# Kernel tuning notes

Hardware: AMD Instinct MI355X
Metric: run time of the kernel (lower is better)

The kernel has to match this reference:

```python
import jax, jax.numpy as jnp
import numpy as np

D = 1024  # input_size
NORM = 1.0 / np.sqrt(D)


def setup_inputs() -> dict:
    key = jax.random.key(0)
    k_x, k_q, k_k, k_v = jax.random.split(key, 4)
    B, S = 4, 2048
    scale = 1.0 / np.sqrt(D)  # init ~ nn.Linear default magnitude
    return {
        "inputs": jax.random.normal(k_x, (B, S, D), dtype=jnp.float32),
        "Wq": jax.random.uniform(k_q, (D, D), jnp.float32, -scale, scale),
        "Wk": jax.random.uniform(k_k, (D, D), jnp.float32, -scale, scale),
        "Wv": jax.random.uniform(k_v, (D, D), jnp.float32, -scale, scale),
    }


def reference(inputs, Wq, Wk, Wv):
    # nn.Linear(x) = x @ W.T (no bias)
    Q = jnp.einsum("bsd,ed->bse", inputs, Wq)
    K = jnp.einsum("bsd,ed->bse", inputs, Wk)
    V = jnp.einsum("bsd,ed->bse", inputs, Wv)
    attn = jnp.einsum("bqe,bke->bqk", Q, K) * NORM  # [B,S,S]
    attn = jax.nn.softmax(attn, axis=2)
    return jnp.einsum("bqk,bke->bqe", attn, V)
```

## Files before the change

### kernel.cpp

```cpp
#include <hip/hip_runtime.h>

typedef __bf16 bf16_t;
typedef __bf16 bf16x8 __attribute__((ext_vector_type(8)));
typedef __bf16 bf16x4 __attribute__((ext_vector_type(4)));
typedef float  floatx4 __attribute__((ext_vector_type(4)));

__device__ __forceinline__ void gload_lds16(const bf16_t* g, bf16_t* l) {
    __builtin_amdgcn_global_load_lds(
        (const __attribute__((address_space(1))) void*)g,
        (__attribute__((address_space(3))) void*)l,
        16, 0, 0);
}

template <int MODE, typename OutT>
__global__ __launch_bounds__(512, 2) void gemm8p(
    const bf16_t* __restrict__ A, int lda, size_t batchA,
    const bf16_t* __restrict__ B, int ldb, size_t batchB,
    OutT* __restrict__ C, int ldc, size_t batchC,
    bf16_t* __restrict__ C2, int ldc2,
    float* __restrict__ rowsums, int batchR,
    int K, float scale)
{
    extern __shared__ __align__(16) bf16_t smem[];

    A += (size_t)blockIdx.z * batchA;
    B += (size_t)blockIdx.z * batchB;

    const int tid  = threadIdx.x;
    const int wid  = tid >> 6;
    const int lane = tid & 63;
    const int wr   = wid >> 2;
    const int wc   = wid & 3;
    const int lr   = lane & 15;

    const int bm = blockIdx.x * 256;
    const int bn = blockIdx.y * 256;

    const bf16_t* At = A + (size_t)bm * lda;
    const bf16_t* Bt = B + (size_t)bn * ldb;

    const int    c8 = (((lane & 3) ^ ((lane >> 3) & 3)) << 3);
    const size_t ga = (size_t)(wid * 16 + (lane >> 2)) * lda + c8;
    const size_t gb = (size_t)(wid * 16 + (lane >> 2)) * ldb + c8;
    bf16_t* lw = smem + (wid << 9);

    const int slotoff = (((lane >> 4) ^ ((lr >> 1) & 3)) << 3);

    const int NT = K >> 6;

    floatx4 acc[8][4] = {};
    bf16x8 af[4], bq[4];

#define STAGE(sbuf, sreg, tile) do {                                          \
    bf16_t* _l = lw + ((((sbuf) << 2) | (sreg)) << 13);                       \
    const size_t _k = (size_t)(tile) * 64 + ((sreg) & 1) * 32;                \
    if ((sreg) >= 2) {                                                        \
        gload_lds16(Bt + _k + gb, _l);                                        \
        gload_lds16(Bt + _k + gb + (size_t)128 * ldb, _l + 4096);             \
    } else {                                                                  \
        gload_lds16(At + _k + ga, _l);                                        \
        gload_lds16(At + _k + ga + (size_t)128 * lda, _l + 4096);             \
    }                                                                         \
} while (0)

#define LDA_FRAG(buf, kk, row)                                                \
    (*(const bf16x8*)&smem[((((buf) << 2) | (kk)) << 13) + ((row) << 5) + slotoff])
#define LDB_FRAG(buf, kk, row)                                                \
    (*(const bf16x8*)&smem[((((buf) << 2) | (2 + (kk))) << 13) + ((row) << 5) + slotoff])

#define PHASE(buf, kk, mh, RDB, sbuf, sreg, stile, DOVM) do {                 \
    if (RDB) {                                                                \
        _Pragma("unroll")                                                     \
        for (int j = 0; j < 4; ++j)                                           \
            bq[j] = LDB_FRAG(buf, kk, wc * 64 + j * 16 + lr);                 \
    }                                                                         \
    _Pragma("unroll")                                                         \
    for (int i = 0; i < 4; ++i)                                               \
        af[i] = LDA_FRAG(buf, kk, wr * 128 + (mh) * 64 + i * 16 + lr);        \
    STAGE(sbuf, sreg, stile);                                                 \
    if (DOVM) asm volatile("s_waitcnt vmcnt(6)" ::: "memory");                \
    __builtin_amdgcn_s_barrier();                                             \
    __builtin_amdgcn_s_setprio(1);                                            \
    _Pragma("unroll")                                                         \
    for (int i = 0; i < 4; ++i) {                                             \
        _Pragma("unroll")                                                     \
        for (int j = 0; j < 4; ++j)                                           \
            acc[(mh) * 4 + i][j] = __builtin_amdgcn_mfma_f32_16x16x32_bf16(   \
                bq[j], af[i], acc[(mh) * 4 + i][j], 0, 0, 0);                 \
    }                                                                         \
    __builtin_amdgcn_s_setprio(0);                                            \
    __builtin_amdgcn_s_barrier();                                             \
} while (0)

    STAGE(0, 2, 0); STAGE(0, 0, 0); STAGE(0, 3, 0); STAGE(0, 1, 0);
    STAGE(1, 2, 1); STAGE(1, 0, 1); STAGE(1, 3, 1);
    asm volatile("s_waitcnt vmcnt(6)" ::: "memory");
    __builtin_amdgcn_s_barrier();

    for (int kt = 0; kt < NT; kt += 2) {
        int t1 = kt + 1;
        int t2 = kt + 2; if (t2 >= NT) t2 -= NT;
        int t3 = kt + 3; if (t3 >= NT) t3 -= NT;
        PHASE(0, 0, 0, true,  1, 1, t1, false);
        PHASE(0, 0, 1, false, 0, 2, t2, false);
        PHASE(0, 1, 0, true,  0, 0, t2, false);
        PHASE(0, 1, 1, false, 0, 3, t2, true);
        PHASE(1, 0, 0, true,  0, 1, t2, false);
        PHASE(1, 0, 1, false, 1, 2, t3, false);
        PHASE(1, 1, 0, true,  1, 0, t3, false);
        PHASE(1, 1, 1, false, 1, 3, t3, true);
    }
    asm volatile("s_waitcnt vmcnt(0)" ::: "memory");

#undef PHASE
#undef LDA_FRAG
#undef LDB_FRAG
#undef STAGE

    const int cfix = lane & 15;
    const int creg = (lane >> 4) << 2;

    if constexpr (MODE == 1) {
        if (blockIdx.z == 2) {
            #pragma unroll
            for (int mi = 0; mi < 8; ++mi) {
                int mg = bm + wr * 128 + mi * 16 + cfix;
                #pragma unroll
                for (int j = 0; j < 4; ++j) {
                    int ng = bn + wc * 64 + j * 16 + creg;
                    #pragma unroll
                    for (int r = 0; r < 4; ++r)
                        C2[(size_t)(ng + r) * ldc2 + mg] = (bf16_t)acc[mi][j][r];
                }
            }
            return;
        }
        OutT* Cz = C + (size_t)blockIdx.z * batchC;
        #pragma unroll
        for (int mi = 0; mi < 8; ++mi) {
            size_t row = (size_t)(bm + wr * 128 + mi * 16 + cfix);
            #pragma unroll
            for (int j = 0; j < 4; ++j) {
                int col = bn + wc * 64 + j * 16 + creg;
                bf16x4 v;
                #pragma unroll
                for (int r = 0; r < 4; ++r) v[r] = (bf16_t)acc[mi][j][r];
                *(bf16x4*)&Cz[row * (size_t)ldc + col] = v;
            }
        }
    } else {
        OutT* Cz = C + (size_t)blockIdx.z * batchC;
        float* sums = rowsums + (size_t)blockIdx.z * batchR;
        float rs[8] = {};
        #pragma unroll
        for (int mi = 0; mi < 8; ++mi) {
            size_t row = (size_t)(bm + wr * 128 + mi * 16 + cfix);
            #pragma unroll
            for (int j = 0; j < 4; ++j) {
                int col = bn + wc * 64 + j * 16 + creg;
                bf16x4 v;
                #pragma unroll
                for (int r = 0; r < 4; ++r) {
                    v[r] = (bf16_t)__expf(acc[mi][j][r] * scale);
                    rs[mi] += (float)v[r];
                }
                *(bf16x4*)&Cz[row * (size_t)ldc + col] = v;
            }
        }
        #pragma unroll
        for (int mi = 0; mi < 8; ++mi) {
            rs[mi] += __shfl_xor(rs[mi], 16);
            rs[mi] += __shfl_xor(rs[mi], 32);
        }
        if (lane < 16) {
            #pragma unroll
            for (int mi = 0; mi < 8; ++mi)
                atomicAdd(&sums[bm + wr * 128 + mi * 16 + lane], rs[mi]);
        }
    }
}

template <int MODE, int BKT, typename OutT>
__global__ __launch_bounds__(256) void gemm_nt(
    const bf16_t* __restrict__ A, int lda, size_t batchA,
    const bf16_t* __restrict__ B, int ldb, size_t batchB,
    OutT* __restrict__ C, int ldc, size_t batchC,
    bf16_t* __restrict__ C2, int ldc2,
    float* __restrict__ rowsums, int batchR,
    int K, float scale)
{
    constexpr int CH  = BKT / 8;
    constexpr int RPS = 2048 / BKT;
    constexpr int NSHOT = 128 / RPS;

    __shared__ bf16_t sA[128 * BKT];
    __shared__ bf16_t sB[128 * BKT];

    A += (size_t)blockIdx.z * batchA;
    B += (size_t)blockIdx.z * batchB;

    const int tid  = threadIdx.x;
    const int wid  = tid >> 6;
    const int lane = tid & 63;

    const int bm = blockIdx.x * 128;
    const int bn = blockIdx.y * 128;

    const int rr  = tid / CH;
    const int kc8 = (((tid & (CH - 1)) ^ (rr & (CH - 1))) << 3);

    const int wy = (wid >> 1) * 64;
    const int wx = (wid & 1) * 64;
    const int lr = lane & 15;

    floatx4 acc[4][4] = {};

    const bf16_t* pa = A + (size_t)(bm + rr) * lda + kc8;
    const bf16_t* pb = B + (size_t)(bn + rr) * ldb + kc8;
    bf16_t* la = &sA[wid * 512];
    bf16_t* lb = &sB[wid * 512];

    for (int k0 = 0; k0 < K; k0 += BKT) {
        #pragma unroll
        for (int c = 0; c < NSHOT; ++c) {
            gload_lds16(pa + (size_t)(c * RPS) * lda + k0, la + c * 2048);
            gload_lds16(pb + (size_t)(c * RPS) * ldb + k0, lb + c * 2048);
        }
        __syncthreads();

        #pragma unroll
        for (int kk = 0; kk < BKT / 32; ++kk) {
            const int cch = (kk << 2) + (lane >> 4);
            bf16x8 af[4], bqf[4];
            #pragma unroll
            for (int i = 0; i < 4; ++i) {
                int r = wy + i * 16 + lr;
                af[i] = *(const bf16x8*)&sA[r * BKT + ((cch ^ (r & (CH - 1))) << 3)];
            }
            #pragma unroll
            for (int j = 0; j < 4; ++j) {
                int r = wx + j * 16 + lr;
                bqf[j] = *(const bf16x8*)&sB[r * BKT + ((cch ^ (r & (CH - 1))) << 3)];
            }
            #pragma unroll
            for (int i = 0; i < 4; ++i)
                #pragma unroll
                for (int j = 0; j < 4; ++j)
                    acc[i][j] = __builtin_amdgcn_mfma_f32_16x16x32_bf16(
                        bqf[j], af[i], acc[i][j], 0, 0, 0);
        }
        __syncthreads();
    }

    const int cfix = lane & 15;
    const int creg = (lane >> 4) << 2;

    if constexpr (MODE == 3) {
        OutT* Cz = C + (size_t)blockIdx.z * batchC;
        const float* sums = rowsums + (size_t)blockIdx.z * batchR;
        #pragma unroll
        for (int i = 0; i < 4; ++i) {
            int rloc = bm + wy + i * 16 + cfix;
            float rinv = 1.0f / sums[rloc];
            size_t row = (size_t)rloc;
            #pragma unroll
            for (int j = 0; j < 4; ++j) {
                int col = bn + wx + j * 16 + creg;
                floatx4 v;
                #pragma unroll
                for (int r = 0; r < 4; ++r) v[r] = acc[i][j][r] * rinv;
                *(floatx4*)&Cz[row * (size_t)ldc + col] = v;
            }
        }
    }
    (void)C2; (void)ldc2; (void)scale;
}

__global__ __launch_bounds__(256) void cvt_all(
    const float* __restrict__ X, const float* __restrict__ Wq,
    const float* __restrict__ Wk, const float* __restrict__ Wv,
    bf16_t* __restrict__ Xb, bf16_t* __restrict__ Wqb,
    bf16_t* __restrict__ Wkb, bf16_t* __restrict__ Wvb,
    float* __restrict__ sums, int nsums,
    int nX4, int nW4)
{
    int i = blockIdx.x * blockDim.x + threadIdx.x;
    if (i < nsums) sums[i] = 0.f;
    const float* src; bf16_t* dst; int idx;
    if (i < nX4) { src = X; dst = Xb; idx = i; }
    else {
        int j = i - nX4;
        int w = j / nW4;
        idx = j - w * nW4;
        if (i >= nX4 + 3 * nW4) return;
        src = (w == 0) ? Wq : (w == 1) ? Wk : Wv;
        dst = (w == 0) ? Wqb : (w == 1) ? Wkb : Wvb;
    }
    float4 v = ((const float4*)src)[idx];
    bf16x4 o;
    o[0] = (bf16_t)v.x; o[1] = (bf16_t)v.y; o[2] = (bf16_t)v.z; o[3] = (bf16_t)v.w;
    *(bf16x4*)(dst + (size_t)idx * 4) = o;
}

extern "C" void kernel_launch(void* const* d_in, const int* in_sizes, int n_in,
                              void* d_out, int out_size, void* d_ws, size_t ws_size,
                              hipStream_t stream)
{
    (void)in_sizes; (void)n_in; (void)out_size; (void)ws_size;
    const float* X  = (const float*)d_in[0];
    const float* Wq = (const float*)d_in[1];
    const float* Wk = (const float*)d_in[2];
    const float* Wv = (const float*)d_in[3];
    float* out = (float*)d_out;

    const int Bb = 4, S = 2048, D = 1024;
    const int M = Bb * S;

    char* ws = (char*)d_ws;
    size_t off = 0;
    auto carve = [&](size_t bytes) -> char* {
        char* p = ws + off;
        off += (bytes + 255) & ~(size_t)255;
        return p;
    };
    bf16_t* Xb  = (bf16_t*)carve((size_t)M * D * 2);
    bf16_t* Wqb = (bf16_t*)carve((size_t)D * D * 2);
    bf16_t* Wkb = (bf16_t*)carve((size_t)D * D * 2);
    bf16_t* Wvb = (bf16_t*)carve((size_t)D * D * 2);
    bf16_t* Qb  = (bf16_t*)carve((size_t)M * D * 2);
    bf16_t* Kb  = (bf16_t*)carve((size_t)M * D * 2);
    bf16_t* Vt  = (bf16_t*)carve((size_t)D * M * 2);
    bf16_t* Sc  = (bf16_t*)carve((size_t)Bb * S * S * 2);
    float*  sums = (float*)carve((size_t)M * 4);

    static bool s_attr = false;
    if (!s_attr) {
        (void)hipFuncSetAttribute(
            reinterpret_cast<const void*>(&gemm8p<1, bf16_t>),
            hipFuncAttributeMaxDynamicSharedMemorySize, 131072);
        (void)hipFuncSetAttribute(
            reinterpret_cast<const void*>(&gemm8p<2, bf16_t>),
            hipFuncAttributeMaxDynamicSharedMemorySize, 131072);
        s_attr = true;
    }

    const int nX4 = M * D / 4, nW4 = D * D / 4;
    const int tot4 = nX4 + 3 * nW4;
    cvt_all<<<(tot4 + 255) / 256, 256, 0, stream>>>(
        X, Wq, Wk, Wv, Xb, Wqb, Wkb, Wvb, sums, M, nX4, nW4);

    gemm8p<1, bf16_t><<<dim3(M / 256, D / 256, 3), 512, 131072, stream>>>(
        Xb, D, 0, Wqb, D, (size_t)D * D, Qb, D, (size_t)M * D,
        Vt, M, nullptr, 0, D, 1.0f);

    gemm8p<2, bf16_t><<<dim3(S / 256, S / 256, Bb), 512, 131072, stream>>>(
        Qb, D, (size_t)S * D, Kb, D, (size_t)S * D, Sc, S, (size_t)S * S,
        nullptr, 0, sums, S, D, 0.03125f);

    gemm_nt<3, 128, float><<<dim3(S / 128, D / 128, Bb), 256, 0, stream>>>(
        Sc, S, (size_t)S * S, Vt, M, (size_t)S, out, D, (size_t)S * D,
        nullptr, 0, sums, S, S, 1.0f);
}
```

Measured before the change: 234.5 us.

## Fuse Q/K projections into one interleaved GEMM and split V-transpose into separate kernel

The Q and K projections now run as a single GEMM with N=2D over contiguous Wq/Wk weights, writing an interleaved [M, 2D] buffer that the score GEMM reads with a doubled leading dimension. The transposed V projection moves out of the big 256-tile kernel into a new mode of the smaller 128-tile gemm_nt kernel, which removes the per-block branch and the scattered transposed store from the main projection kernel. The cost is one extra kernel launch, and the V projection now runs on a smaller tile configuration that may be less efficient. The score GEMM's operand reads are strided across the wider interleaved rows.

```diff
diff --git a/kernel.cpp b/kernel.cpp
--- a/kernel.cpp
+++ b/kernel.cpp
@@ -17,7 +17,6 @@
     const bf16_t* __restrict__ A, int lda, size_t batchA,
     const bf16_t* __restrict__ B, int ldb, size_t batchB,
     OutT* __restrict__ C, int ldc, size_t batchC,
-    bf16_t* __restrict__ C2, int ldc2,
     float* __restrict__ rowsums, int batchR,
     int K, float scale)
 {
@@ -121,20 +120,6 @@
     const int creg = (lane >> 4) << 2;
 
     if constexpr (MODE == 1) {
-        if (blockIdx.z == 2) {
-            #pragma unroll
-            for (int mi = 0; mi < 8; ++mi) {
-                int mg = bm + wr * 128 + mi * 16 + cfix;
-                #pragma unroll
-                for (int j = 0; j < 4; ++j) {
-                    int ng = bn + wc * 64 + j * 16 + creg;
-                    #pragma unroll
-                    for (int r = 0; r < 4; ++r)
-                        C2[(size_t)(ng + r) * ldc2 + mg] = (bf16_t)acc[mi][j][r];
-                }
-            }
-            return;
-        }
         OutT* Cz = C + (size_t)blockIdx.z * batchC;
         #pragma unroll
         for (int mi = 0; mi < 8; ++mi) {
@@ -272,8 +257,21 @@
                 *(floatx4*)&Cz[row * (size_t)ldc + col] = v;
             }
         }
-    }
-    (void)C2; (void)ldc2; (void)scale;
+    } else if constexpr (MODE == 4) {
+        #pragma unroll
+        for (int i = 0; i < 4; ++i) {
+            int mg = bm + wy + i * 16 + cfix;
+            #pragma unroll
+            for (int j = 0; j < 4; ++j) {
+                int ng = bn + wx + j * 16 + creg;
+                #pragma unroll
+                for (int r = 0; r < 4; ++r)
+                    C2[(size_t)(ng + r) * ldc2 + mg] = (bf16_t)acc[i][j][r];
+            }
+        }
+    }
+    (void)C; (void)ldc; (void)batchC; (void)C2; (void)ldc2;
+    (void)rowsums; (void)batchR; (void)scale;
 }
 
 __global__ __launch_bounds__(256) void cvt_all(
@@ -327,8 +325,7 @@
     bf16_t* Wqb = (bf16_t*)carve((size_t)D * D * 2);
     bf16_t* Wkb = (bf16_t*)carve((size_t)D * D * 2);
     bf16_t* Wvb = (bf16_t*)carve((size_t)D * D * 2);
-    bf16_t* Qb  = (bf16_t*)carve((size_t)M * D * 2);
-    bf16_t* Kb  = (bf16_t*)carve((size_t)M * D * 2);
+    bf16_t* QKb = (bf16_t*)carve((size_t)M * 2 * D * 2);
     bf16_t* Vt  = (bf16_t*)carve((size_t)D * M * 2);
     bf16_t* Sc  = (bf16_t*)carve((size_t)Bb * S * S * 2);
     float*  sums = (float*)carve((size_t)M * 4);
@@ -349,13 +346,17 @@
     cvt_all<<<(tot4 + 255) / 256, 256, 0, stream>>>(
         X, Wq, Wk, Wv, Xb, Wqb, Wkb, Wvb, sums, M, nX4, nW4);
 
-    gemm8p<1, bf16_t><<<dim3(M / 256, D / 256, 3), 512, 131072, stream>>>(
-        Xb, D, 0, Wqb, D, (size_t)D * D, Qb, D, (size_t)M * D,
+    gemm8p<1, bf16_t><<<dim3(M / 256, (2 * D) / 256, 1), 512, 131072, stream>>>(
+        Xb, D, 0, Wqb, D, 0, QKb, 2 * D, 0,
+        nullptr, 0, D, 1.0f);
+
+    gemm_nt<4, 64, bf16_t><<<dim3(M / 128, D / 128, 1), 256, 0, stream>>>(
+        Xb, D, 0, Wvb, D, 0, nullptr, 0, 0,
         Vt, M, nullptr, 0, D, 1.0f);
 
     gemm8p<2, bf16_t><<<dim3(S / 256, S / 256, Bb), 512, 131072, stream>>>(
-        Qb, D, (size_t)S * D, Kb, D, (size_t)S * D, Sc, S, (size_t)S * S,
-        nullptr, 0, sums, S, D, 0.03125f);
+        QKb, 2 * D, (size_t)S * 2 * D, QKb + D, 2 * D, (size_t)S * 2 * D,
+        Sc, S, (size_t)S * S, sums, S, D, 0.03125f);
 
     gemm_nt<3, 128, float><<<dim3(S / 128, D / 128, Bb), 256, 0, stream>>>(
         Sc, S, (size_t)S * S, Vt, M, (size_t)S, out, D, (size_t)S * D,
```

Result: no change. 234.4 us (-0.0%).

## Generalize pipelined GEMM over tile width and use it for V and PV

Applied to the files above, without the earlier changes.

Adds a tile-width template parameter (256 or 128 columns) to the 8-wave pipelined GEMM and resizes its LDS regions and vmcnt waits to match. The Q and K projections now run as one GEMM over the stacked Wq/Wk weights. V-transpose is computed directly as Wv·Xᵀ, which replaces the scattered transposed stores. The simple non-pipelined PV kernel is replaced by the pipelined kernel with 256x128 tiles. This removes uncoalesced transpose writes and gives the final GEMM the double-buffered schedule. In exchange it relies on Wqb/Wkb and Qb/Kb being laid out back to back in the workspace.

```diff
diff --git a/kernel.cpp b/kernel.cpp
--- a/kernel.cpp
+++ b/kernel.cpp
@@ -12,16 +12,25 @@
         16, 0, 0);
 }
 
-template <int MODE, typename OutT>
+template <int MODE, int BN, typename OutT>
 __global__ __launch_bounds__(512, 2) void gemm8p(
     const bf16_t* __restrict__ A, int lda, size_t batchA,
     const bf16_t* __restrict__ B, int ldb, size_t batchB,
     OutT* __restrict__ C, int ldc, size_t batchC,
-    bf16_t* __restrict__ C2, int ldc2,
+    bf16_t* __restrict__ C2,
     float* __restrict__ rowsums, int batchR,
     int K, float scale)
 {
     extern __shared__ __align__(16) bf16_t smem[];
+
+    constexpr int NJ   = BN / 64;
+    constexpr int WCB  = BN / 4;
+    constexpr int BGL  = BN / 128;
+    constexpr int AREG = 8192;
+    constexpr int BREG = BN * 32;
+    constexpr int BOFF = 2 * AREG;
+    constexpr int BUFS = BOFF + 2 * BREG;
+    constexpr int VM   = 2 + 2 * BGL;
 
     A += (size_t)blockIdx.z * batchA;
     B += (size_t)blockIdx.z * batchB;
@@ -34,7 +43,7 @@
     const int lr   = lane & 15;
 
     const int bm = blockIdx.x * 256;
-    const int bn = blockIdx.y * 256;
+    const int bn = blockIdx.y * BN;
 
     const bf16_t* At = A + (size_t)bm * lda;
     const bf16_t* Bt = B + (size_t)bn * ldb;
@@ -42,21 +51,24 @@
     const int    c8 = (((lane & 3) ^ ((lane >> 3) & 3)) << 3);
     const size_t ga = (size_t)(wid * 16 + (lane >> 2)) * lda + c8;
     const size_t gb = (size_t)(wid * 16 + (lane >> 2)) * ldb + c8;
-    bf16_t* lw = smem + (wid << 9);
 
     const int slotoff = (((lane >> 4) ^ ((lr >> 1) & 3)) << 3);
 
     const int NT = K >> 6;
 
-    floatx4 acc[8][4] = {};
-    bf16x8 af[4], bq[4];
+    floatx4 acc[8][NJ] = {};
+    bf16x8 af[4], bq[NJ];
+
+#define RBASE(sbuf, sreg)                                                     \
+    ((sbuf) * BUFS + ((sreg) < 2 ? (sreg) * AREG : BOFF + ((sreg) - 2) * BREG))
 
 #define STAGE(sbuf, sreg, tile) do {                                          \
-    bf16_t* _l = lw + ((((sbuf) << 2) | (sreg)) << 13);                       \
+    bf16_t* _l = smem + RBASE(sbuf, sreg) + (wid << 9);                       \
     const size_t _k = (size_t)(tile) * 64 + ((sreg) & 1) * 32;                \
     if ((sreg) >= 2) {                                                        \
         gload_lds16(Bt + _k + gb, _l);                                        \
-        gload_lds16(Bt + _k + gb + (size_t)128 * ldb, _l + 4096);             \
+        if (BGL == 2)                                                         \
+            gload_lds16(Bt + _k + gb + (size_t)128 * ldb, _l + 4096);         \
     } else {                                                                  \
         gload_lds16(At + _k + ga, _l);                                        \
         gload_lds16(At + _k + ga + (size_t)128 * lda, _l + 4096);             \
@@ -64,27 +76,30 @@
 } while (0)
 
 #define LDA_FRAG(buf, kk, row)                                                \
-    (*(const bf16x8*)&smem[((((buf) << 2) | (kk)) << 13) + ((row) << 5) + slotoff])
+    (*(const bf16x8*)&smem[(buf) * BUFS + (kk) * AREG + ((row) << 5) + slotoff])
 #define LDB_FRAG(buf, kk, row)                                                \
-    (*(const bf16x8*)&smem[((((buf) << 2) | (2 + (kk))) << 13) + ((row) << 5) + slotoff])
+    (*(const bf16x8*)&smem[(buf) * BUFS + BOFF + (kk) * BREG + ((row) << 5) + slotoff])
 
 #define PHASE(buf, kk, mh, RDB, sbuf, sreg, stile, DOVM) do {                 \
     if (RDB) {                                                                \
         _Pragma("unroll")                                                     \
-        for (int j = 0; j < 4; ++j)                                           \
-            bq[j] = LDB_FRAG(buf, kk, wc * 64 + j * 16 + lr);                 \
+        for (int j = 0; j < NJ; ++j)                                          \
+            bq[j] = LDB_FRAG(buf, kk, wc * WCB + j * 16 + lr);                \
     }                                                                         \
     _Pragma("unroll")                                                         \
     for (int i = 0; i < 4; ++i)                                               \
         af[i] = LDA_FRAG(buf, kk, wr * 128 + (mh) * 64 + i * 16 + lr);        \
     STAGE(sbuf, sreg, stile);                                                 \
-    if (DOVM) asm volatile("s_waitcnt vmcnt(6)" ::: "memory");                \
+    if (DOVM) {                                                               \
+        if constexpr (VM == 6) asm volatile("s_waitcnt vmcnt(6)" ::: "memory");\
+        else                   asm volatile("s_waitcnt vmcnt(4)" ::: "memory");\
+    }                                                                         \
     __builtin_amdgcn_s_barrier();                                             \
     __builtin_amdgcn_s_setprio(1);                                            \
     _Pragma("unroll")                                                         \
     for (int i = 0; i < 4; ++i) {                                             \
         _Pragma("unroll")                                                     \
-        for (int j = 0; j < 4; ++j)                                           \
+        for (int j = 0; j < NJ; ++j)                                          \
             acc[(mh) * 4 + i][j] = __builtin_amdgcn_mfma_f32_16x16x32_bf16(   \
                 bq[j], af[i], acc[(mh) * 4 + i][j], 0, 0, 0);                 \
     }                                                                         \
@@ -94,7 +109,8 @@
 
     STAGE(0, 2, 0); STAGE(0, 0, 0); STAGE(0, 3, 0); STAGE(0, 1, 0);
     STAGE(1, 2, 1); STAGE(1, 0, 1); STAGE(1, 3, 1);
-    asm volatile("s_waitcnt vmcnt(6)" ::: "memory");
+    if constexpr (VM == 6) asm volatile("s_waitcnt vmcnt(6)" ::: "memory");
+    else                   asm volatile("s_waitcnt vmcnt(4)" ::: "memory");
     __builtin_amdgcn_s_barrier();
 
     for (int kt = 0; kt < NT; kt += 2) {
@@ -116,39 +132,41 @@
 #undef LDA_FRAG
 #undef LDB_FRAG
 #undef STAGE
+#undef RBASE
 
     const int cfix = lane & 15;
     const int creg = (lane >> 4) << 2;
 
     if constexpr (MODE == 1) {
-        if (blockIdx.z == 2) {
-            #pragma unroll
-            for (int mi = 0; mi < 8; ++mi) {
-                int mg = bm + wr * 128 + mi * 16 + cfix;
-                #pragma unroll
-                for (int j = 0; j < 4; ++j) {
-                    int ng = bn + wc * 64 + j * 16 + creg;
-                    #pragma unroll
-                    for (int r = 0; r < 4; ++r)
-                        C2[(size_t)(ng + r) * ldc2 + mg] = (bf16_t)acc[mi][j][r];
-                }
-            }
-            return;
-        }
         OutT* Cz = C + (size_t)blockIdx.z * batchC;
         #pragma unroll
         for (int mi = 0; mi < 8; ++mi) {
             size_t row = (size_t)(bm + wr * 128 + mi * 16 + cfix);
             #pragma unroll
-            for (int j = 0; j < 4; ++j) {
-                int col = bn + wc * 64 + j * 16 + creg;
+            for (int j = 0; j < NJ; ++j) {
+                int col = bn + wc * WCB + j * 16 + creg;
                 bf16x4 v;
                 #pragma unroll
                 for (int r = 0; r < 4; ++r) v[r] = (bf16_t)acc[mi][j][r];
                 *(bf16x4*)&Cz[row * (size_t)ldc + col] = v;
             }
         }
-    } else {
+    } else if constexpr (MODE == 5) {
+        bf16_t* dst = (bn < 1024) ? (bf16_t*)C : C2;
+        const int cb = bn & 1023;
+        #pragma unroll
+        for (int mi = 0; mi < 8; ++mi) {
+            size_t row = (size_t)(bm + wr * 128 + mi * 16 + cfix);
+            #pragma unroll
+            for (int j = 0; j < NJ; ++j) {
+                int col = cb + wc * WCB + j * 16 + creg;
+                bf16x4 v;
+                #pragma unroll
+                for (int r = 0; r < 4; ++r) v[r] = (bf16_t)acc[mi][j][r];
+                *(bf16x4*)&dst[row * (size_t)ldc + col] = v;
+            }
+        }
+    } else if constexpr (MODE == 2) {
         OutT* Cz = C + (size_t)blockIdx.z * batchC;
         float* sums = rowsums + (size_t)blockIdx.z * batchR;
         float rs[8] = {};
@@ -156,8 +174,8 @@
         for (int mi = 0; mi < 8; ++mi) {
             size_t row = (size_t)(bm + wr * 128 + mi * 16 + cfix);
             #pragma unroll
-            for (int j = 0; j < 4; ++j) {
-                int col = bn + wc * 64 + j * 16 + creg;
+            for (int j = 0; j < NJ; ++j) {
+                int col = bn + wc * WCB + j * 16 + creg;
                 bf16x4 v;
                 #pragma unroll
                 for (int r = 0; r < 4; ++r) {
@@ -177,103 +195,24 @@
             for (int mi = 0; mi < 8; ++mi)
                 atomicAdd(&sums[bm + wr * 128 + mi * 16 + lane], rs[mi]);
         }
-    }
-}
-
-template <int MODE, int BKT, typename OutT>
-__global__ __launch_bounds__(256) void gemm_nt(
-    const bf16_t* __restrict__ A, int lda, size_t batchA,
-    const bf16_t* __restrict__ B, int ldb, size_t batchB,
-    OutT* __restrict__ C, int ldc, size_t batchC,
-    bf16_t* __restrict__ C2, int ldc2,
-    float* __restrict__ rowsums, int batchR,
-    int K, float scale)
-{
-    constexpr int CH  = BKT / 8;
-    constexpr int RPS = 2048 / BKT;
-    constexpr int NSHOT = 128 / RPS;
-
-    __shared__ bf16_t sA[128 * BKT];
-    __shared__ bf16_t sB[128 * BKT];
-
-    A += (size_t)blockIdx.z * batchA;
-    B += (size_t)blockIdx.z * batchB;
-
-    const int tid  = threadIdx.x;
-    const int wid  = tid >> 6;
-    const int lane = tid & 63;
-
-    const int bm = blockIdx.x * 128;
-    const int bn = blockIdx.y * 128;
-
-    const int rr  = tid / CH;
-    const int kc8 = (((tid & (CH - 1)) ^ (rr & (CH - 1))) << 3);
-
-    const int wy = (wid >> 1) * 64;
-    const int wx = (wid & 1) * 64;
-    const int lr = lane & 15;
-
-    floatx4 acc[4][4] = {};
-
-    const bf16_t* pa = A + (size_t)(bm + rr) * lda + kc8;
-    const bf16_t* pb = B + (size_t)(bn + rr) * ldb + kc8;
-    bf16_t* la = &sA[wid * 512];
-    bf16_t* lb = &sB[wid * 512];
-
-    for (int k0 = 0; k0 < K; k0 += BKT) {
-        #pragma unroll
-        for (int c = 0; c < NSHOT; ++c) {
-            gload_lds16(pa + (size_t)(c * RPS) * lda + k0, la + c * 2048);
-            gload_lds16(pb + (size_t)(c * RPS) * ldb + k0, lb + c * 2048);
-        }
-        __syncthreads();
-
-        #pragma unroll
-        for (int kk = 0; kk < BKT / 32; ++kk) {
-            const int cch = (kk << 2) + (lane >> 4);
-            bf16x8 af[4], bqf[4];
-            #pragma unroll
-            for (int i = 0; i < 4; ++i) {
-                int r = wy + i * 16 + lr;
-                af[i] = *(const bf16x8*)&sA[r * BKT + ((cch ^ (r & (CH - 1))) << 3)];
-            }
-            #pragma unroll
-            for (int j = 0; j < 4; ++j) {
-                int r = wx + j * 16 + lr;
-                bqf[j] = *(const bf16x8*)&sB[r * BKT + ((cch ^ (r & (CH - 1))) << 3)];
-            }
-            #pragma unroll
-            for (int i = 0; i < 4; ++i)
-                #pragma unroll
-                for (int j = 0; j < 4; ++j)
-                    acc[i][j] = __builtin_amdgcn_mfma_f32_16x16x32_bf16(
-                        bqf[j], af[i], acc[i][j], 0, 0, 0);
-        }
-        __syncthreads();
-    }
-
-    const int cfix = lane & 15;
-    const int creg = (lane >> 4) << 2;
-
-    if constexpr (MODE == 3) {
+    } else {
         OutT* Cz = C + (size_t)blockIdx.z * batchC;
         const float* sums = rowsums + (size_t)blockIdx.z * batchR;
         #pragma unroll
-        for (int i = 0; i < 4; ++i) {
-            int rloc = bm + wy + i * 16 + cfix;
+        for (int mi = 0; mi < 8; ++mi) {
+            int rloc = bm + wr * 128 + mi * 16 + cfix;
             float rinv = 1.0f / sums[rloc];
             size_t row = (size_t)rloc;
             #pragma unroll
-            for (int j = 0; j < 4; ++j) {
-                int col = bn + wx + j * 16 + creg;
+            for (int j = 0; j < NJ; ++j) {
+                int col = bn + wc * WCB + j * 16 + creg;
                 floatx4 v;
                 #pragma unroll
-                for (int r = 0; r < 4; ++r) v[r] = acc[i][j][r] * rinv;
+                for (int r = 0; r < 4; ++r) v[r] = acc[mi][j][r] * rinv;
                 *(floatx4*)&Cz[row * (size_t)ldc + col] = v;
             }
         }
     }
-    (void)C2; (void)ldc2; (void)scale;
 }
 
 __global__ __launch_bounds__(256) void cvt_all(
@@ -336,11 +275,17 @@
     static bool s_attr = false;
     if (!s_attr) {
         (void)hipFuncSetAttribute(
-            reinterpret_cast<const void*>(&gemm8p<1, bf16_t>),
+            reinterpret_cast<const void*>(&gemm8p<5, 256, bf16_t>),
             hipFuncAttributeMaxDynamicSharedMemorySize, 131072);
         (void)hipFuncSetAttribute(
-            reinterpret_cast<const void*>(&gemm8p<2, bf16_t>),
+            reinterpret_cast<const void*>(&gemm8p<2, 256, bf16_t>),
             hipFuncAttributeMaxDynamicSharedMemorySize, 131072);
+        (void)hipFuncSetAttribute(
+            reinterpret_cast<const void*>(&gemm8p<1, 128, bf16_t>),
+            hipFuncAttributeMaxDynamicSharedMemorySize, 98304);
+        (void)hipFuncSetAttribute(
+            reinterpret_cast<const void*>(&gemm8p<3, 128, float>),
+            hipFuncAttributeMaxDynamicSharedMemorySize, 98304);
         s_attr = true;
     }
 
@@ -349,15 +294,17 @@
     cvt_all<<<(tot4 + 255) / 256, 256, 0, stream>>>(
         X, Wq, Wk, Wv, Xb, Wqb, Wkb, Wvb, sums, M, nX4, nW4);
 
-    gemm8p<1, bf16_t><<<dim3(M / 256, D / 256, 3), 512, 131072, stream>>>(
-        Xb, D, 0, Wqb, D, (size_t)D * D, Qb, D, (size_t)M * D,
-        Vt, M, nullptr, 0, D, 1.0f);
-
-    gemm8p<2, bf16_t><<<dim3(S / 256, S / 256, Bb), 512, 131072, stream>>>(
+    gemm8p<5, 256, bf16_t><<<dim3(M / 256, (2 * D) / 256, 1), 512, 131072, stream>>>(
+        Xb, D, 0, Wqb, D, 0, Qb, D, 0, Kb, nullptr, 0, D, 1.0f);
+
+    gemm8p<1, 128, bf16_t><<<dim3(D / 256, M / 128, 1), 512, 98304, stream>>>(
+        Wvb, D, 0, Xb, D, 0, Vt, M, 0, nullptr, nullptr, 0, D, 1.0f);
+
+    gemm8p<2, 256, bf16_t><<<dim3(S / 256, S / 256, Bb), 512, 131072, stream>>>(
         Qb, D, (size_t)S * D, Kb, D, (size_t)S * D, Sc, S, (size_t)S * S,
-        nullptr, 0, sums, S, D, 0.03125f);
-
-    gemm_nt<3, 128, float><<<dim3(S / 128, D / 128, Bb), 256, 0, stream>>>(
+        nullptr, sums, S, D, 0.03125f);
+
+    gemm8p<3, 128, float><<<dim3(S / 256, D / 128, Bb), 512, 98304, stream>>>(
         Sc, S, (size_t)S * S, Vt, M, (size_t)S, out, D, (size_t)S * D,
-        nullptr, 0, sums, S, S, 1.0f);
+        nullptr, sums, S, S, 1.0f);
 }
```

Result: no change. 230.7 us (-1.6%).
